# Optimization experiments

Measured on AMD Instinct MI355X. Metric: run time of the kernel, lower is better.

## Reference

```python
import jax, jax.numpy as jnp
import numpy as np

F_NODES = 360        # nodes per graph == num_features (square connectome)
NUM_GRAPHS = 128
NUM_EDGES = 1_000_000
C = 128              # hidden_channels
NUM_LAYERS = 3
HIDDEN = 512
NUM_CLASSES = 2
EPS = 1e-5


def _bn(x, g, b):
    # BatchNorm1d in training mode: biased batch statistics over the batch dim.
    m = x.mean(axis=0)
    v = x.var(axis=0)
    return (x - m) * jax.lax.rsqrt(v + EPS) * g + b


def _gcn(x, W, b, src, dst):
    # GCNConv: x' = D^{-1/2} (A + I) D^{-1/2} (x W) + b
    N = x.shape[0]
    h = x @ W                                   # [N, C]
    loop = jnp.arange(N, dtype=src.dtype)
    src2 = jnp.concatenate([src, loop])
    dst2 = jnp.concatenate([dst, loop])
    deg = jax.ops.segment_sum(jnp.ones_like(dst2, dtype=h.dtype), dst2, num_segments=N)
    dinv = jnp.where(deg > 0, jax.lax.rsqrt(deg), 0.0)
    norm = dinv[src2] * dinv[dst2]              # [E+N]
    out = jax.ops.segment_sum(h[src2] * norm[:, None], dst2, num_segments=N)
    return out + b


def setup_inputs() -> dict:
    key = jax.random.key(0)
    ks = jax.random.split(key, 16)
    N = NUM_GRAPHS * F_NODES
    x = jax.random.normal(ks[0], (N, F_NODES), jnp.float32)
    # edges confined within each graph
    g = jax.random.randint(ks[1], (NUM_EDGES,), 0, NUM_GRAPHS)
    edge_src = g * F_NODES + jax.random.randint(ks[2], (NUM_EDGES,), 0, F_NODES)
    edge_dst = g * F_NODES + jax.random.randint(ks[3], (NUM_EDGES,), 0, F_NODES)
    batch = jnp.repeat(jnp.arange(NUM_GRAPHS), F_NODES)

    def lin(k, fi, fo):
        s = 1.0 / np.sqrt(fi)
        return jax.random.uniform(k, (fi, fo), jnp.float32, -s, s)

    input_dim = F_NODES * (F_NODES + 1) // 2    # 64980
    input_dim1 = input_dim + C * NUM_LAYERS     # 65364
    H2 = HIDDEN // 2
    params = dict(
        Wc1=lin(ks[4], F_NODES, C), bc1=jnp.zeros((C,), jnp.float32),
        Wc2=lin(ks[5], C, C), bc2=jnp.zeros((C,), jnp.float32),
        Wc3=lin(ks[6], C, C), bc3=jnp.zeros((C,), jnp.float32),
        bn_g=jnp.ones((input_dim,), jnp.float32), bn_b=jnp.zeros((input_dim,), jnp.float32),
        bnh_g=jnp.ones((C * NUM_LAYERS,), jnp.float32), bnh_b=jnp.zeros((C * NUM_LAYERS,), jnp.float32),
        W1=lin(ks[7], input_dim1, HIDDEN), b1=jnp.zeros((HIDDEN,), jnp.float32),
        g1=jnp.ones((HIDDEN,), jnp.float32), be1=jnp.zeros((HIDDEN,), jnp.float32),
        W2=lin(ks[8], HIDDEN, H2), b2=jnp.zeros((H2,), jnp.float32),
        g2=jnp.ones((H2,), jnp.float32), be2=jnp.zeros((H2,), jnp.float32),
        W3=lin(ks[9], H2, H2), b3=jnp.zeros((H2,), jnp.float32),
        g3=jnp.ones((H2,), jnp.float32), be3=jnp.zeros((H2,), jnp.float32),
        W4=lin(ks[10], H2, NUM_CLASSES), b4=jnp.zeros((NUM_CLASSES,), jnp.float32),
    )
    return {"x": x, "edge_src": edge_src, "edge_dst": edge_dst, "batch": batch, **params}


def reference(x, edge_src, edge_dst, batch,
              Wc1, bc1, Wc2, bc2, Wc3, bc3,
              bn_g, bn_b, bnh_g, bnh_b,
              W1, b1, g1, be1, W2, b2, g2, be2, W3, b3, g3, be3, W4, b4):
    N, F = x.shape
    B = N // F                                   # nodes per graph == F
    # stacked GCN convs with tanh
    xs = [x]
    for W, b in ((Wc1, bc1), (Wc2, bc2), (Wc3, bc3)):
        xs.append(jnp.tanh(_gcn(xs[-1], W, b, edge_src, edge_dst)))
    # per-graph upper-triangular gather of the raw connectome (vectorized)
    iu0, iu1 = np.triu_indices(F)
    x0 = xs[0].reshape(B, F, F)[:, iu0, iu1]     # [B, F(F+1)/2]
    x0 = _bn(x0, bn_g, bn_b)
    # per-layer segment-mean pooling over graphs
    cnt = jax.ops.segment_sum(jnp.ones((N,), x.dtype), batch, num_segments=B)
    h = jnp.concatenate(
        [jax.ops.segment_sum(xx, batch, num_segments=B) / cnt[:, None] for xx in xs[1:]],
        axis=1)                                  # [B, C*num_layers]
    h = _bn(h, bnh_g, bnh_b)
    z = jnp.concatenate([x0, h], axis=1)         # [B, input_dim1]
    # MLP head (dropout in eval mode => identity)
    z = jax.nn.relu(_bn(z @ W1 + b1, g1, be1))
    z = jax.nn.relu(_bn(z @ W2 + b2, g2, be2))
    z = jax.nn.relu(_bn(z @ W3 + b3, g3, be3))
    return jax.nn.log_softmax(z @ W4 + b4, axis=1)
```

## Files before the change

### kernel.cpp

```cpp
#include <hip/hip_runtime.h>
#include <hip/hip_bf16.h>
#include <math.h>

#define FN 360
#define NG 128
#define NN 46080
#define CH 128
#define NE 1000000
#define TRI 64980
#define D1 65364
#define ZLD 65376
#define H1 512
#define H2 256
#define EPS 1e-5f
#define NSPLIT 128

typedef unsigned short u16;
typedef __attribute__((ext_vector_type(8))) short bf16x8;
typedef __attribute__((ext_vector_type(4))) float f32x4;

__device__ __forceinline__ float bf2f(u16 v) {
  union { unsigned u; float f; } x; x.u = ((unsigned)v) << 16; return x.f;
}
__device__ __forceinline__ u16 f2bf(float f) {
  union { float f; unsigned u; } x; x.f = f;
  unsigned r = x.u + 0x7fffu + ((x.u >> 16) & 1u);
  return (u16)(r >> 16);
}
__device__ __forceinline__ bf16x8 bzero8() {
  bf16x8 z;
#pragma unroll
  for (int j = 0; j < 8; j++) z[j] = 0;
  return z;
}

static const size_t A32_OFF  = 0;
static const size_t Z_OFF    = 0;
static const size_t PART_OFF = 16736256;
static const size_t Y1_OFF   = 50290688;
static const size_t A1_OFF   = 50552832;
static const size_t A2_OFF   = 50683904;
static const size_t A3_OFF   = 50749440;
static const size_t DEG_OFF  = 66355200;
static const size_t HP_OFF   = 66539520;
static const size_t AB_OFF   = 66736128;
static const size_t PT_OFF   = 99913728;
static const size_t H_OFF    = 111710208;

__global__ void k_deg(const int* __restrict__ dst, float* __restrict__ deg) {
  int e = blockIdx.x * 256 + threadIdx.x;
  if (e < NE) atomicAdd(&deg[dst[e]], 1.0f);
}

__global__ void k_abuild(const int* __restrict__ src, const int* __restrict__ dst,
                         const float* __restrict__ deg, float* __restrict__ A) {
  int e = blockIdx.x * 256 + threadIdx.x;
  if (e < NE) {
    int s = src[e], d = dst[e];
    int g = d / FN;
    int ls = s - g * FN, ld = d - g * FN;
    float w = rsqrtf(deg[s] + 1.0f) * rsqrtf(deg[d] + 1.0f);
    atomicAdd(&A[(size_t)g * FN * FN + (size_t)ld * FN + ls], w);
  } else if (e < NE + NN) {
    int i = e - NE;
    int g = i / FN, l = i - g * FN;
    float dv = rsqrtf(deg[i] + 1.0f);
    atomicAdd(&A[(size_t)g * FN * FN + (size_t)l * FN + l], dv * dv);
  }
}

__global__ __launch_bounds__(256) void k_gemm_xw_f32(
    const float* __restrict__ X, const float* __restrict__ W,
    u16* __restrict__ PT, int K) {
  __shared__ __attribute__((aligned(16))) u16 WT[128][40];
  int wid = threadIdx.x >> 6, lane = threadIdx.x & 63;
  int quad = lane >> 4, l16 = lane & 15;
  int m0 = blockIdx.x * 64 + (wid & 1) * 32;
  int n0w = (wid >> 1) * 64;
  int kl = threadIdx.x >> 3, nseg = (threadIdx.x & 7) * 16;
  f32x4 acc[2][4];
#pragma unroll
  for (int i = 0; i < 2; i++)
#pragma unroll
    for (int j = 0; j < 4; j++) acc[i][j] = (f32x4){0,0,0,0};
  for (int k0 = 0; k0 < K; k0 += 32) {
    __syncthreads();
    int kg = k0 + kl;
    if (kg < K) {
      const float* wrow = W + (size_t)kg * CH + nseg;
      f32x4 w0 = *(const f32x4*)(wrow);
      f32x4 w1 = *(const f32x4*)(wrow + 4);
      f32x4 w2 = *(const f32x4*)(wrow + 8);
      f32x4 w3 = *(const f32x4*)(wrow + 12);
#pragma unroll
      for (int j = 0; j < 4; j++) {
        WT[nseg + j][kl]      = f2bf(w0[j]);
        WT[nseg + 4 + j][kl]  = f2bf(w1[j]);
        WT[nseg + 8 + j][kl]  = f2bf(w2[j]);
        WT[nseg + 12 + j][kl] = f2bf(w3[j]);
      }
    } else {
#pragma unroll
      for (int j = 0; j < 16; j++) WT[nseg + j][kl] = 0;
    }
    __syncthreads();
    int kk = k0 + quad * 8;
    bool kin = kk < K;
    bf16x8 af[2];
#pragma unroll
    for (int tm = 0; tm < 2; tm++) {
      int row = m0 + tm * 16 + l16;
      bf16x8 a = bzero8();
      if (kin) {
        f32x4 va = *(const f32x4*)(X + (size_t)row * K + kk);
        f32x4 vb = *(const f32x4*)(X + (size_t)row * K + kk + 4);
#pragma unroll
        for (int j = 0; j < 4; j++) { a[j] = (short)f2bf(va[j]); a[4 + j] = (short)f2bf(vb[j]); }
      }
      af[tm] = a;
    }
    bf16x8 bfr[4];
#pragma unroll
    for (int tn = 0; tn < 4; tn++)
      bfr[tn] = *(const bf16x8*)&WT[n0w + tn * 16 + l16][quad * 8];
#pragma unroll
    for (int tm = 0; tm < 2; tm++)
#pragma unroll
      for (int tn = 0; tn < 4; tn++)
        acc[tm][tn] = __builtin_amdgcn_mfma_f32_16x16x32_bf16(af[tm], bfr[tn], acc[tm][tn], 0, 0, 0);
  }
#pragma unroll
  for (int tm = 0; tm < 2; tm++)
#pragma unroll
    for (int tn = 0; tn < 4; tn++) {
      int col = n0w + tn * 16 + l16;
      int rowb = m0 + tm * 16 + quad * 4;
#pragma unroll
      for (int r = 0; r < 4; r++) {
        int row = rowb + r;
        int g = row / FN, lr = row - g * FN;
        PT[((size_t)g * CH + col) * FN + lr] = f2bf(acc[tm][tn][r]);
      }
    }
}

__global__ __launch_bounds__(256) void k_gemm_xw_bf16(
    const u16* __restrict__ X, const float* __restrict__ W,
    u16* __restrict__ PT) {
  __shared__ __attribute__((aligned(16))) u16 WT[128][40];
  int wid = threadIdx.x >> 6, lane = threadIdx.x & 63;
  int quad = lane >> 4, l16 = lane & 15;
  int m0 = blockIdx.x * 64 + (wid & 1) * 32;
  int n0w = (wid >> 1) * 64;
  int kl = threadIdx.x >> 3, nseg = (threadIdx.x & 7) * 16;
  f32x4 acc[2][4];
#pragma unroll
  for (int i = 0; i < 2; i++)
#pragma unroll
    for (int j = 0; j < 4; j++) acc[i][j] = (f32x4){0,0,0,0};
  for (int k0 = 0; k0 < CH; k0 += 32) {
    __syncthreads();
    int kg = k0 + kl;
    const float* wrow = W + (size_t)kg * CH + nseg;
    f32x4 w0 = *(const f32x4*)(wrow);
    f32x4 w1 = *(const f32x4*)(wrow + 4);
    f32x4 w2 = *(const f32x4*)(wrow + 8);
    f32x4 w3 = *(const f32x4*)(wrow + 12);
#pragma unroll
    for (int j = 0; j < 4; j++) {
      WT[nseg + j][kl]      = f2bf(w0[j]);
      WT[nseg + 4 + j][kl]  = f2bf(w1[j]);
      WT[nseg + 8 + j][kl]  = f2bf(w2[j]);
      WT[nseg + 12 + j][kl] = f2bf(w3[j]);
    }
    __syncthreads();
    int kk = k0 + quad * 8;
    bf16x8 af[2];
#pragma unroll
    for (int tm = 0; tm < 2; tm++) {
      int row = m0 + tm * 16 + l16;
      af[tm] = *(const bf16x8*)(X + (size_t)row * CH + kk);
    }
    bf16x8 bfr[4];
#pragma unroll
    for (int tn = 0; tn < 4; tn++)
      bfr[tn] = *(const bf16x8*)&WT[n0w + tn * 16 + l16][quad * 8];
#pragma unroll
    for (int tm = 0; tm < 2; tm++)
#pragma unroll
      for (int tn = 0; tn < 4; tn++)
        acc[tm][tn] = __builtin_amdgcn_mfma_f32_16x16x32_bf16(af[tm], bfr[tn], acc[tm][tn], 0, 0, 0);
  }
#pragma unroll
  for (int tm = 0; tm < 2; tm++)
#pragma unroll
    for (int tn = 0; tn < 4; tn++) {
      int col = n0w + tn * 16 + l16;
      int rowb = m0 + tm * 16 + quad * 4;
#pragma unroll
      for (int r = 0; r < 4; r++) {
        int row = rowb + r;
        int g = row / FN, lr = row - g * FN;
        PT[((size_t)g * CH + col) * FN + lr] = f2bf(acc[tm][tn][r]);
      }
    }
}

__global__ __launch_bounds__(256) void k_agg1(
    const float* __restrict__ A32, const u16* __restrict__ PT,
    const float* __restrict__ bias, u16* __restrict__ Hout,
    u16* __restrict__ Ab, float* __restrict__ hp) {
  __shared__ float ps[8][128];
  int id = blockIdx.x;
  int g = (id & 7) + 8 * (id / 48);
  int mb = (id % 48) >> 3;
  int wid = threadIdx.x >> 6, lane = threadIdx.x & 63;
  int quad = lane >> 4, l16 = lane & 15;
  int m0 = mb * 64 + (wid & 1) * 32;
  int n0 = (wid >> 1) * 64;
  const float* Ag = A32 + (size_t)g * FN * FN;
  u16* Abg = Ab + (size_t)g * FN * FN;
  const u16* PTg = PT + (size_t)g * CH * FN;
  bool wr_ab = ((wid >> 1) == 0);
  f32x4 acc[2][4];
#pragma unroll
  for (int i = 0; i < 2; i++)
#pragma unroll
    for (int j = 0; j < 4; j++) acc[i][j] = (f32x4){0,0,0,0};
  for (int k0 = 0; k0 < FN; k0 += 32) {
    int kk = k0 + quad * 8;
    bool kin = kk < FN;
    bf16x8 af[2];
#pragma unroll
    for (int tm = 0; tm < 2; tm++) {
      int row = m0 + tm * 16 + l16;
      bf16x8 a = bzero8();
      if (kin && row < FN) {
        f32x4 va = *(const f32x4*)(Ag + (size_t)row * FN + kk);
        f32x4 vb = *(const f32x4*)(Ag + (size_t)row * FN + kk + 4);
#pragma unroll
        for (int j = 0; j < 4; j++) { a[j] = (short)f2bf(va[j]); a[4 + j] = (short)f2bf(vb[j]); }
        if (wr_ab) *(bf16x8*)(Abg + (size_t)row * FN + kk) = a;
      }
      af[tm] = a;
    }
    bf16x8 bfr[4];
#pragma unroll
    for (int tn = 0; tn < 4; tn++) {
      int col = n0 + tn * 16 + l16;
      bfr[tn] = kin ? *(const bf16x8*)(PTg + (size_t)col * FN + kk) : bzero8();
    }
#pragma unroll
    for (int tm = 0; tm < 2; tm++)
#pragma unroll
      for (int tn = 0; tn < 4; tn++)
        acc[tm][tn] = __builtin_amdgcn_mfma_f32_16x16x32_bf16(af[tm], bfr[tn], acc[tm][tn], 0, 0, 0);
  }
  float lsum[4] = {0.f, 0.f, 0.f, 0.f};
#pragma unroll
  for (int tm = 0; tm < 2; tm++)
#pragma unroll
    for (int tn = 0; tn < 4; tn++) {
      int col = n0 + tn * 16 + l16;
      float bc = bias[col];
      int rowb = m0 + tm * 16 + quad * 4;
#pragma unroll
      for (int r = 0; r < 4; r++) {
        int row = rowb + r;
        if (row < FN) {
          float t = tanhf(acc[tm][tn][r] + bc);
          Hout[(size_t)(g * FN + row) * CH + col] = f2bf(t);
          lsum[tn] += t;
        }
      }
    }
  int cid = (wid & 1) * 4 + quad;
#pragma unroll
  for (int tn = 0; tn < 4; tn++) ps[cid][n0 + tn * 16 + l16] = lsum[tn];
  __syncthreads();
  if (threadIdx.x < 128) {
    float s = 0.f;
#pragma unroll
    for (int c = 0; c < 8; c++) s += ps[c][threadIdx.x];
    atomicAdd(&hp[g * 384 + threadIdx.x], s);
  }
}

__global__ __launch_bounds__(256) void k_agg23(
    const u16* __restrict__ Ab, const u16* __restrict__ PT,
    const float* __restrict__ bias, u16* __restrict__ Hout,
    float* __restrict__ hp, int loff) {
  __shared__ float ps[8][128];
  int id = blockIdx.x;
  int g = (id & 7) + 8 * (id / 48);
  int mb = (id % 48) >> 3;
  int wid = threadIdx.x >> 6, lane = threadIdx.x & 63;
  int quad = lane >> 4, l16 = lane & 15;
  int m0 = mb * 64 + (wid & 1) * 32;
  int n0 = (wid >> 1) * 64;
  const u16* Abg = Ab + (size_t)g * FN * FN;
  const u16* PTg = PT + (size_t)g * CH * FN;
  f32x4 acc[2][4];
#pragma unroll
  for (int i = 0; i < 2; i++)
#pragma unroll
    for (int j = 0; j < 4; j++) acc[i][j] = (f32x4){0,0,0,0};
  for (int k0 = 0; k0 < FN; k0 += 32) {
    int kk = k0 + quad * 8;
    bool kin = kk < FN;
    bf16x8 af[2];
#pragma unroll
    for (int tm = 0; tm < 2; tm++) {
      int row = m0 + tm * 16 + l16;
      af[tm] = (kin && row < FN) ? *(const bf16x8*)(Abg + (size_t)row * FN + kk) : bzero8();
    }
    bf16x8 bfr[4];
#pragma unroll
    for (int tn = 0; tn < 4; tn++) {
      int col = n0 + tn * 16 + l16;
      bfr[tn] = kin ? *(const bf16x8*)(PTg + (size_t)col * FN + kk) : bzero8();
    }
#pragma unroll
    for (int tm = 0; tm < 2; tm++)
#pragma unroll
      for (int tn = 0; tn < 4; tn++)
        acc[tm][tn] = __builtin_amdgcn_mfma_f32_16x16x32_bf16(af[tm], bfr[tn], acc[tm][tn], 0, 0, 0);
  }
  float lsum[4] = {0.f, 0.f, 0.f, 0.f};
#pragma unroll
  for (int tm = 0; tm < 2; tm++)
#pragma unroll
    for (int tn = 0; tn < 4; tn++) {
      int col = n0 + tn * 16 + l16;
      float bc = bias[col];
      int rowb = m0 + tm * 16 + quad * 4;
#pragma unroll
      for (int r = 0; r < 4; r++) {
        int row = rowb + r;
        if (row < FN) {
          float t = tanhf(acc[tm][tn][r] + bc);
          if (Hout) Hout[(size_t)(g * FN + row) * CH + col] = f2bf(t);
          lsum[tn] += t;
        }
      }
    }
  int cid = (wid & 1) * 4 + quad;
#pragma unroll
  for (int tn = 0; tn < 4; tn++) ps[cid][n0 + tn * 16 + l16] = lsum[tn];
  __syncthreads();
  if (threadIdx.x < 128) {
    float s = 0.f;
#pragma unroll
    for (int c = 0; c < 8; c++) s += ps[c][threadIdx.x];
    atomicAdd(&hp[g * 384 + loff + threadIdx.x], s);
  }
}

__global__ __launch_bounds__(256) void k_gemm_big(
    const u16* __restrict__ Z, const float* __restrict__ W1f, float* __restrict__ part) {
  __shared__ __attribute__((aligned(16))) u16 WT[128][40];
  int id = blockIdx.x;
  int s = (id & 7) + 8 * (id >> 5);
  int n0b = ((id >> 3) & 3) * 128;
  int wid = threadIdx.x >> 6, lane = threadIdx.x & 63;
  int quad = lane >> 4, l16 = lane & 15;
  int m0 = wid * 32;
  int kl = threadIdx.x >> 3, nseg = (threadIdx.x & 7) * 16;
  int kbeg = s * 512;
  int kend = (ZLD < kbeg + 512) ? ZLD : (kbeg + 512);
  f32x4 acc[2][8];
#pragma unroll
  for (int i = 0; i < 2; i++)
#pragma unroll
    for (int j = 0; j < 8; j++) acc[i][j] = (f32x4){0,0,0,0};
  for (int k0 = kbeg; k0 < kend; k0 += 32) {
    __syncthreads();
    int kg = k0 + kl;
    if (kg < D1) {
      const float* wrow = W1f + (size_t)kg * H1 + n0b + nseg;
      f32x4 w0 = *(const f32x4*)(wrow);
      f32x4 w1 = *(const f32x4*)(wrow + 4);
      f32x4 w2 = *(const f32x4*)(wrow + 8);
      f32x4 w3 = *(const f32x4*)(wrow + 12);
#pragma unroll
      for (int j = 0; j < 4; j++) {
        WT[nseg + j][kl]      = f2bf(w0[j]);
        WT[nseg + 4 + j][kl]  = f2bf(w1[j]);
        WT[nseg + 8 + j][kl]  = f2bf(w2[j]);
        WT[nseg + 12 + j][kl] = f2bf(w3[j]);
      }
    } else {
#pragma unroll
      for (int j = 0; j < 16; j++) WT[nseg + j][kl] = 0;
    }
    __syncthreads();
    int kk = k0 + quad * 8;
    bf16x8 af[2];
#pragma unroll
    for (int tm = 0; tm < 2; tm++) {
      int row = m0 + tm * 16 + l16;
      af[tm] = *(const bf16x8*)(Z + (size_t)row * ZLD + kk);
    }
    bf16x8 bfr[8];
#pragma unroll
    for (int tn = 0; tn < 8; tn++)
      bfr[tn] = *(const bf16x8*)&WT[tn * 16 + l16][quad * 8];
#pragma unroll
    for (int tm = 0; tm < 2; tm++)
#pragma unroll
      for (int tn = 0; tn < 8; tn++)
        acc[tm][tn] = __builtin_amdgcn_mfma_f32_16x16x32_bf16(af[tm], bfr[tn], acc[tm][tn], 0, 0, 0);
  }
#pragma unroll
  for (int tm = 0; tm < 2; tm++)
#pragma unroll
    for (int tn = 0; tn < 8; tn++) {
      int col = n0b + tn * 16 + l16;
      int rowb = m0 + tm * 16 + quad * 4;
#pragma unroll
      for (int r = 0; r < 4; r++)
        part[((size_t)s * NG + rowb + r) * H1 + col] = acc[tm][tn][r];
    }
}

__global__ void k_red(const float* __restrict__ part, float* __restrict__ y1) {
  int idx = blockIdx.x * 256 + threadIdx.x;
  float s = 0.f;
#pragma unroll 8
  for (int i = 0; i < NSPLIT; i++) s += part[(size_t)i * 65536 + idx];
  y1[idx] = s;
}

__global__ __launch_bounds__(256) void k_bnrelu(
    const float* __restrict__ y, const float* __restrict__ gam,
    const float* __restrict__ bet, u16* __restrict__ a, int N) {
  __shared__ float sb[4][64], sb2[4][64];
  int c63 = threadIdx.x & 63;
  int grp = threadIdx.x >> 6;
  int c = blockIdx.x * 64 + c63;
  float s = 0.f, ss = 0.f;
#pragma unroll 8
  for (int m = grp * 32; m < grp * 32 + 32; m++) {
    float v = y[(size_t)m * N + c]; s += v; ss += v * v;
  }
  sb[grp][c63] = s; sb2[grp][c63] = ss;
  __syncthreads();
  float S = sb[0][c63] + sb[1][c63] + sb[2][c63] + sb[3][c63];
  float SS = sb2[0][c63] + sb2[1][c63] + sb2[2][c63] + sb2[3][c63];
  float mean = S * (1.0f / NG);
  float var = fmaxf(SS * (1.0f / NG) - mean * mean, 0.f);
  float rstd = rsqrtf(var + EPS);
  float ga = gam[c] * rstd;
  float bb = bet[c] - mean * ga;
#pragma unroll 8
  for (int m = grp * 32; m < grp * 32 + 32; m++) {
    float v = y[(size_t)m * N + c] * ga + bb;
    a[(size_t)m * N + c] = f2bf(fmaxf(v, 0.f));
  }
}

__global__ __launch_bounds__(256) void k_mlpbn(
    const u16* __restrict__ A, const float* __restrict__ W,
    const float* __restrict__ gam, const float* __restrict__ bet,
    u16* __restrict__ aout, int K, int N) {
  __shared__ __attribute__((aligned(16))) u16 WT[64][40];
  __shared__ float rs[4][4][4][16], rss[4][4][4][16];
  int wid = threadIdx.x >> 6, lane = threadIdx.x & 63;
  int quad = lane >> 4, l16 = lane & 15;
  int n0b = blockIdx.x * 64;
  int m0 = wid * 32;
  int kl = threadIdx.x >> 3;
  int nseg = (threadIdx.x & 7) * 8;
  f32x4 acc[2][4];
#pragma unroll
  for (int i = 0; i < 2; i++)
#pragma unroll
    for (int j = 0; j < 4; j++) acc[i][j] = (f32x4){0,0,0,0};
  for (int k0 = 0; k0 < K; k0 += 32) {
    __syncthreads();
    const float* wrow = W + (size_t)(k0 + kl) * N + n0b + nseg;
    f32x4 w0 = *(const f32x4*)(wrow);
    f32x4 w1 = *(const f32x4*)(wrow + 4);
#pragma unroll
    for (int j = 0; j < 4; j++) {
      WT[nseg + j][kl]     = f2bf(w0[j]);
      WT[nseg + 4 + j][kl] = f2bf(w1[j]);
    }
    __syncthreads();
    int kk = k0 + quad * 8;
    bf16x8 af[2];
#pragma unroll
    for (int tm = 0; tm < 2; tm++) {
      int row = m0 + tm * 16 + l16;
      af[tm] = *(const bf16x8*)(A + (size_t)row * K + kk);
    }
    bf16x8 bfr[4];
#pragma unroll
    for (int tn = 0; tn < 4; tn++)
      bfr[tn] = *(const bf16x8*)&WT[tn * 16 + l16][quad * 8];
#pragma unroll
    for (int tm = 0; tm < 2; tm++)
#pragma unroll
      for (int tn = 0; tn < 4; tn++)
        acc[tm][tn] = __builtin_amdgcn_mfma_f32_16x16x32_bf16(af[tm], bfr[tn], acc[tm][tn], 0, 0, 0);
  }
  __syncthreads();
#pragma unroll
  for (int tn = 0; tn < 4; tn++) {
    float s = 0.f, ss = 0.f;
#pragma unroll
    for (int tm = 0; tm < 2; tm++)
#pragma unroll
      for (int r = 0; r < 4; r++) { float v = acc[tm][tn][r]; s += v; ss += v * v; }
    rs[wid][quad][tn][l16] = s;
    rss[wid][quad][tn][l16] = ss;
  }
  __syncthreads();
#pragma unroll
  for (int tn = 0; tn < 4; tn++) {
    float S = 0.f, SS = 0.f;
#pragma unroll
    for (int w = 0; w < 4; w++)
#pragma unroll
      for (int q = 0; q < 4; q++) { S += rs[w][q][tn][l16]; SS += rss[w][q][tn][l16]; }
    float mean = S * (1.0f / NG);
    float var = fmaxf(SS * (1.0f / NG) - mean * mean, 0.f);
    float rstd = rsqrtf(var + EPS);
    int col = n0b + tn * 16 + l16;
    float ga = gam[col] * rstd;
    float bb = bet[col] - mean * ga;
#pragma unroll
    for (int tm = 0; tm < 2; tm++) {
      int rowb = m0 + tm * 16 + quad * 4;
#pragma unroll
      for (int r = 0; r < 4; r++) {
        float v = acc[tm][tn][r] * ga + bb;
        aout[(size_t)(rowb + r) * N + col] = f2bf(fmaxf(v, 0.f));
      }
    }
  }
}

__global__ __launch_bounds__(256) void k_x0bn(
    const float* __restrict__ x, const float* __restrict__ gam,
    const float* __restrict__ bet, const float* __restrict__ hp,
    const float* __restrict__ hgam, const float* __restrict__ hbet,
    u16* __restrict__ z) {
  int i = blockIdx.x;
  if (i < FN) {
    int off = i * FN - (i * (i - 1)) / 2;
    for (int j = i + (int)threadIdx.x; j < FN; j += 256) {
      float s = 0.f, ss = 0.f;
#pragma unroll 8
      for (int b = 0; b < NG; b++) {
        float v = x[(size_t)(b * FN + i) * FN + j];
        s += v; ss += v * v;
      }
      float mean = s * (1.0f / NG);
      float var = fmaxf(ss * (1.0f / NG) - mean * mean, 0.f);
      float rstd = rsqrtf(var + EPS);
      int f = off + (j - i);
      float ga = gam[f] * rstd;
      float bb = bet[f] - mean * ga;
#pragma unroll 8
      for (int b = 0; b < NG; b++) {
        float v = x[(size_t)(b * FN + i) * FN + j];
        z[(size_t)b * ZLD + f] = f2bf(v * ga + bb);
      }
    }
  } else {
    for (int c = threadIdx.x; c < 384; c += 256) {
      float s = 0.f, ss = 0.f;
#pragma unroll 8
      for (int m = 0; m < NG; m++) {
        float v = hp[m * 384 + c] * (1.0f / FN);
        s += v; ss += v * v;
      }
      float mean = s * (1.0f / NG);
      float var = fmaxf(ss * (1.0f / NG) - mean * mean, 0.f);
      float rstd = rsqrtf(var + EPS);
      float ga = hgam[c] * rstd;
      float bb = hbet[c] - mean * ga;
#pragma unroll 8
      for (int m = 0; m < NG; m++)
        z[(size_t)m * ZLD + TRI + c] = f2bf(hp[m * 384 + c] * (1.0f / FN) * ga + bb);
    }
    if (threadIdx.x < NG) {
      for (int t = 0; t < ZLD - D1; t++)
        z[(size_t)threadIdx.x * ZLD + D1 + t] = 0;
    }
  }
}

__global__ void k_head(const u16* __restrict__ a3, const float* __restrict__ W4,
                       const float* __restrict__ b4, float* __restrict__ out) {
  __shared__ float w4s[H2 * 2];
  int m = threadIdx.x;
  for (int i = m; i < H2 * 2; i += 128) w4s[i] = W4[i];
  __syncthreads();
  float a0 = b4[0], a1 = b4[1];
  for (int k0 = 0; k0 < H2; k0 += 8) {
    bf16x8 v = *(const bf16x8*)(a3 + (size_t)m * H2 + k0);
#pragma unroll
    for (int j = 0; j < 8; j++) {
      float f = bf2f((u16)v[j]);
      a0 += f * w4s[(k0 + j) * 2];
      a1 += f * w4s[(k0 + j) * 2 + 1];
    }
  }
  float mx = fmaxf(a0, a1);
  float lse = mx + logf(expf(a0 - mx) + expf(a1 - mx));
  out[m * 2]     = a0 - lse;
  out[m * 2 + 1] = a1 - lse;
}

extern "C" void kernel_launch(void* const* d_in, const int* in_sizes, int n_in,
                              void* d_out, int out_size, void* d_ws, size_t ws_size,
                              hipStream_t stream) {
  const float* x    = (const float*)d_in[0];
  const int* esrc   = (const int*)d_in[1];
  const int* edst   = (const int*)d_in[2];
  const float* Wc1 = (const float*)d_in[4];  const float* bc1 = (const float*)d_in[5];
  const float* Wc2 = (const float*)d_in[6];  const float* bc2 = (const float*)d_in[7];
  const float* Wc3 = (const float*)d_in[8];  const float* bc3 = (const float*)d_in[9];
  const float* bn_g = (const float*)d_in[10]; const float* bn_b = (const float*)d_in[11];
  const float* bnh_g = (const float*)d_in[12]; const float* bnh_b = (const float*)d_in[13];
  const float* W1 = (const float*)d_in[14];
  const float* g1 = (const float*)d_in[16]; const float* be1 = (const float*)d_in[17];
  const float* W2 = (const float*)d_in[18];
  const float* g2 = (const float*)d_in[20]; const float* be2 = (const float*)d_in[21];
  const float* W3 = (const float*)d_in[22];
  const float* g3 = (const float*)d_in[24]; const float* be3 = (const float*)d_in[25];
  const float* W4 = (const float*)d_in[26]; const float* b4 = (const float*)d_in[27];

  char* ws = (char*)d_ws;
  float* A32  = (float*)(ws + A32_OFF);
  float* deg  = (float*)(ws + DEG_OFF);
  float* hp   = (float*)(ws + HP_OFF);
  u16*   Ab   = (u16*)(ws + AB_OFF);
  u16*   PT   = (u16*)(ws + PT_OFF);
  u16*   h    = (u16*)(ws + H_OFF);
  u16*   z    = (u16*)(ws + Z_OFF);
  float* part = (float*)(ws + PART_OFF);
  float* y1   = (float*)(ws + Y1_OFF);
  u16*   a1   = (u16*)(ws + A1_OFF);
  u16*   a2   = (u16*)(ws + A2_OFF);
  u16*   a3   = (u16*)(ws + A3_OFF);

  (void)hipMemsetAsync(A32, 0, (size_t)NG * FN * FN * 4 + (size_t)NN * 4 + (size_t)NG * 384 * 4, stream);

  dim3 b256(256);
  k_deg<<<dim3((NE + 255) / 256), b256, 0, stream>>>(edst, deg);
  k_abuild<<<dim3((NE + NN + 255) / 256), b256, 0, stream>>>(esrc, edst, deg, A32);

  k_gemm_xw_f32<<<dim3(NN / 64), b256, 0, stream>>>(x, Wc1, PT, FN);
  k_agg1<<<dim3(NG * 6), b256, 0, stream>>>(A32, PT, bc1, h, Ab, hp);
  k_gemm_xw_bf16<<<dim3(NN / 64), b256, 0, stream>>>(h, Wc2, PT);
  k_agg23<<<dim3(NG * 6), b256, 0, stream>>>(Ab, PT, bc2, h, hp, CH);
  k_gemm_xw_bf16<<<dim3(NN / 64), b256, 0, stream>>>(h, Wc3, PT);
  k_agg23<<<dim3(NG * 6), b256, 0, stream>>>(Ab, PT, bc3, (u16*)nullptr, hp, 2 * CH);

  k_x0bn<<<dim3(FN + 1), b256, 0, stream>>>(x, bn_g, bn_b, hp, bnh_g, bnh_b, z);

  k_gemm_big<<<dim3(512), b256, 0, stream>>>(z, W1, part);
  k_red<<<dim3(65536 / 256), b256, 0, stream>>>(part, y1);
  k_bnrelu<<<dim3(H1 / 64), b256, 0, stream>>>(y1, g1, be1, a1, H1);
  k_mlpbn<<<dim3(H2 / 64), b256, 0, stream>>>(a1, W2, g2, be2, a2, H1, H2);
  k_mlpbn<<<dim3(H2 / 64), b256, 0, stream>>>(a2, W3, g3, be3, a3, H2, H2);
  k_head<<<dim3(1), dim3(128), 0, stream>>>(a3, W4, b4, (float*)d_out);
}
```

Measured before the change: 648.7 us.

## Bucket edges per graph, build adjacency in LDS, overlap big GEMM with aggregation

```diff
diff --git a/kernel.cpp b/kernel.cpp
--- a/kernel.cpp
+++ b/kernel.cpp
@@ -13,7 +13,12 @@
 #define H1 512
 #define H2 256
 #define EPS 1e-5f
-#define NSPLIT 128
+#define NSPLIT 64
+#define NB1 720
+#define EBLK 3907
+#define NSB 8
+#define SBCAP 1536
+#define CROWS 45
 
 typedef unsigned short u16;
 typedef __attribute__((ext_vector_type(8))) short bf16x8;
@@ -42,37 +47,32 @@
 static const size_t A2_OFF   = 50683904;
 static const size_t A3_OFF   = 50749440;
 static const size_t DEG_OFF  = 66355200;
-static const size_t HP_OFF   = 66539520;
-static const size_t AB_OFF   = 66736128;
-static const size_t PT_OFF   = 99913728;
-static const size_t H_OFF    = 111710208;
-
-__global__ void k_deg(const int* __restrict__ dst, float* __restrict__ deg) {
-  int e = blockIdx.x * 256 + threadIdx.x;
-  if (e < NE) atomicAdd(&deg[dst[e]], 1.0f);
-}
-
-__global__ void k_abuild(const int* __restrict__ src, const int* __restrict__ dst,
-                         const float* __restrict__ deg, float* __restrict__ A) {
-  int e = blockIdx.x * 256 + threadIdx.x;
-  if (e < NE) {
-    int s = src[e], d = dst[e];
-    int g = d / FN;
-    int ls = s - g * FN, ld = d - g * FN;
-    float w = rsqrtf(deg[s] + 1.0f) * rsqrtf(deg[d] + 1.0f);
-    atomicAdd(&A[(size_t)g * FN * FN + (size_t)ld * FN + ls], w);
-  } else if (e < NE + NN) {
-    int i = e - NE;
-    int g = i / FN, l = i - g * FN;
-    float dv = rsqrtf(deg[i] + 1.0f);
-    atomicAdd(&A[(size_t)g * FN * FN + (size_t)l * FN + l], dv * dv);
-  }
-}
-
-__global__ __launch_bounds__(256) void k_gemm_xw_f32(
+static const size_t CUR_OFF  = 66539520;
+static const size_t HP_OFF   = 66543616;
+static const size_t AB_OFF   = 66740224;
+static const size_t PT_OFF   = 99917824;
+static const size_t H_OFF    = 111714304;
+
+__global__ __launch_bounds__(256) void k_gemm1deg(
     const float* __restrict__ X, const float* __restrict__ W,
-    u16* __restrict__ PT, int K) {
+    u16* __restrict__ PT,
+    const int* __restrict__ src, const int* __restrict__ dst,
+    float* __restrict__ deg, int* __restrict__ cur, unsigned* __restrict__ ebuf) {
+  if (blockIdx.x >= NB1) {
+    int e = (blockIdx.x - NB1) * 256 + threadIdx.x;
+    if (e < NE) {
+      int s = src[e], d = dst[e];
+      atomicAdd(&deg[d], 1.0f);
+      int g = d / FN;
+      int ls = s - g * FN, ld = d - g * FN;
+      int sb = g * NSB + (e & (NSB - 1));
+      int pos = atomicAdd(&cur[sb], 1);
+      if (pos < SBCAP) ebuf[(size_t)sb * SBCAP + pos] = (unsigned)ls | ((unsigned)ld << 16);
+    }
+    return;
+  }
   __shared__ __attribute__((aligned(16))) u16 WT[128][40];
+  const int K = FN;
   int wid = threadIdx.x >> 6, lane = threadIdx.x & 63;
   int quad = lane >> 4, l16 = lane & 15;
   int m0 = blockIdx.x * 64 + (wid & 1) * 32;
@@ -144,66 +144,42 @@
     }
 }
 
-__global__ __launch_bounds__(256) void k_gemm_xw_bf16(
-    const u16* __restrict__ X, const float* __restrict__ W,
-    u16* __restrict__ PT) {
-  __shared__ __attribute__((aligned(16))) u16 WT[128][40];
-  int wid = threadIdx.x >> 6, lane = threadIdx.x & 63;
-  int quad = lane >> 4, l16 = lane & 15;
-  int m0 = blockIdx.x * 64 + (wid & 1) * 32;
-  int n0w = (wid >> 1) * 64;
-  int kl = threadIdx.x >> 3, nseg = (threadIdx.x & 7) * 16;
-  f32x4 acc[2][4];
-#pragma unroll
-  for (int i = 0; i < 2; i++)
-#pragma unroll
-    for (int j = 0; j < 4; j++) acc[i][j] = (f32x4){0,0,0,0};
-  for (int k0 = 0; k0 < CH; k0 += 32) {
-    __syncthreads();
-    int kg = k0 + kl;
-    const float* wrow = W + (size_t)kg * CH + nseg;
-    f32x4 w0 = *(const f32x4*)(wrow);
-    f32x4 w1 = *(const f32x4*)(wrow + 4);
-    f32x4 w2 = *(const f32x4*)(wrow + 8);
-    f32x4 w3 = *(const f32x4*)(wrow + 12);
-#pragma unroll
-    for (int j = 0; j < 4; j++) {
-      WT[nseg + j][kl]      = f2bf(w0[j]);
-      WT[nseg + 4 + j][kl]  = f2bf(w1[j]);
-      WT[nseg + 8 + j][kl]  = f2bf(w2[j]);
-      WT[nseg + 12 + j][kl] = f2bf(w3[j]);
-    }
-    __syncthreads();
-    int kk = k0 + quad * 8;
-    bf16x8 af[2];
-#pragma unroll
-    for (int tm = 0; tm < 2; tm++) {
-      int row = m0 + tm * 16 + l16;
-      af[tm] = *(const bf16x8*)(X + (size_t)row * CH + kk);
-    }
-    bf16x8 bfr[4];
-#pragma unroll
-    for (int tn = 0; tn < 4; tn++)
-      bfr[tn] = *(const bf16x8*)&WT[n0w + tn * 16 + l16][quad * 8];
-#pragma unroll
-    for (int tm = 0; tm < 2; tm++)
-#pragma unroll
-      for (int tn = 0; tn < 4; tn++)
-        acc[tm][tn] = __builtin_amdgcn_mfma_f32_16x16x32_bf16(af[tm], bfr[tn], acc[tm][tn], 0, 0, 0);
-  }
-#pragma unroll
-  for (int tm = 0; tm < 2; tm++)
-#pragma unroll
-    for (int tn = 0; tn < 4; tn++) {
-      int col = n0w + tn * 16 + l16;
-      int rowb = m0 + tm * 16 + quad * 4;
-#pragma unroll
-      for (int r = 0; r < 4; r++) {
-        int row = rowb + r;
-        int g = row / FN, lr = row - g * FN;
-        PT[((size_t)g * CH + col) * FN + lr] = f2bf(acc[tm][tn][r]);
-      }
-    }
+__global__ __launch_bounds__(256) void k_abuild2(
+    const unsigned* __restrict__ ebuf, const int* __restrict__ cur,
+    const float* __restrict__ deg, float* __restrict__ A) {
+  __shared__ __attribute__((aligned(16))) float sA[CROWS * FN];
+  int g = blockIdx.x >> 3, ch = blockIdx.x & 7;
+  int r0 = ch * CROWS;
+  {
+    f32x4* z4 = (f32x4*)sA;
+    for (int i = threadIdx.x; i < CROWS * FN / 4; i += 256) z4[i] = (f32x4){0,0,0,0};
+  }
+  __syncthreads();
+  const float* dg = deg + g * FN;
+#pragma unroll 1
+  for (int sb = 0; sb < NSB; sb++) {
+    int cnt = cur[g * NSB + sb];
+    if (cnt > SBCAP) cnt = SBCAP;
+    const unsigned* eb = ebuf + (size_t)(g * NSB + sb) * SBCAP;
+    for (int i = threadIdx.x; i < cnt; i += 256) {
+      unsigned p = eb[i];
+      int ls = (int)(p & 0xffffu), ld = (int)(p >> 16);
+      int lr = ld - r0;
+      if ((unsigned)lr < (unsigned)CROWS) {
+        float w = rsqrtf(dg[ls] + 1.0f) * rsqrtf(dg[ld] + 1.0f);
+        atomicAdd(&sA[lr * FN + ls], w);
+      }
+    }
+  }
+  if (threadIdx.x < CROWS) {
+    int l = r0 + threadIdx.x;
+    float dv = rsqrtf(dg[l] + 1.0f);
+    atomicAdd(&sA[threadIdx.x * FN + l], dv * dv);
+  }
+  __syncthreads();
+  f32x4* dst4 = (f32x4*)(A + (size_t)g * FN * FN + (size_t)r0 * FN);
+  const f32x4* s4 = (const f32x4*)sA;
+  for (int i = threadIdx.x; i < CROWS * FN / 4; i += 256) dst4[i] = s4[i];
 }
 
 __global__ __launch_bounds__(256) void k_agg1(
@@ -286,10 +262,83 @@
   }
 }
 
+template<bool GUARD>
+__device__ __forceinline__ void gbig_body(
+    const u16* __restrict__ Z, const float* __restrict__ W1f,
+    float* __restrict__ part, int s, int n0b) {
+  __shared__ __attribute__((aligned(16))) u16 WT[128][40];
+  int wid = threadIdx.x >> 6, lane = threadIdx.x & 63;
+  int quad = lane >> 4, l16 = lane & 15;
+  int m0 = wid * 32;
+  int kl = threadIdx.x >> 3, nseg = (threadIdx.x & 7) * 16;
+  int kbeg = s * 1024;
+  int kend = GUARD ? ((ZLD < kbeg + 1024) ? ZLD : (kbeg + 1024)) : (kbeg + 1024);
+  f32x4 acc[2][8];
+#pragma unroll
+  for (int i = 0; i < 2; i++)
+#pragma unroll
+    for (int j = 0; j < 8; j++) acc[i][j] = (f32x4){0,0,0,0};
+  for (int k0 = kbeg; k0 < kend; k0 += 32) {
+    __syncthreads();
+    int kg = k0 + kl;
+    if (!GUARD || kg < D1) {
+      const float* wrow = W1f + (size_t)kg * H1 + n0b + nseg;
+      f32x4 w0 = *(const f32x4*)(wrow);
+      f32x4 w1 = *(const f32x4*)(wrow + 4);
+      f32x4 w2 = *(const f32x4*)(wrow + 8);
+      f32x4 w3 = *(const f32x4*)(wrow + 12);
+#pragma unroll
+      for (int j = 0; j < 4; j++) {
+        WT[nseg + j][kl]      = f2bf(w0[j]);
+        WT[nseg + 4 + j][kl]  = f2bf(w1[j]);
+        WT[nseg + 8 + j][kl]  = f2bf(w2[j]);
+        WT[nseg + 12 + j][kl] = f2bf(w3[j]);
+      }
+    } else {
+#pragma unroll
+      for (int j = 0; j < 16; j++) WT[nseg + j][kl] = 0;
+    }
+    __syncthreads();
+    int kk = k0 + quad * 8;
+    bf16x8 af[2];
+#pragma unroll
+    for (int tm = 0; tm < 2; tm++) {
+      int row = m0 + tm * 16 + l16;
+      af[tm] = *(const bf16x8*)(Z + (size_t)row * ZLD + kk);
+    }
+    bf16x8 bfr[8];
+#pragma unroll
+    for (int tn = 0; tn < 8; tn++)
+      bfr[tn] = *(const bf16x8*)&WT[tn * 16 + l16][quad * 8];
+#pragma unroll
+    for (int tm = 0; tm < 2; tm++)
+#pragma unroll
+      for (int tn = 0; tn < 8; tn++)
+        acc[tm][tn] = __builtin_amdgcn_mfma_f32_16x16x32_bf16(af[tm], bfr[tn], acc[tm][tn], 0, 0, 0);
+  }
+#pragma unroll
+  for (int tm = 0; tm < 2; tm++)
+#pragma unroll
+    for (int tn = 0; tn < 8; tn++) {
+      int col = n0b + tn * 16 + l16;
+      int rowb = m0 + tm * 16 + quad * 4;
+#pragma unroll
+      for (int r = 0; r < 4; r++)
+        part[((size_t)s * NG + rowb + r) * H1 + col] = acc[tm][tn][r];
+    }
+}
+
 __global__ __launch_bounds__(256) void k_agg23(
     const u16* __restrict__ Ab, const u16* __restrict__ PT,
     const float* __restrict__ bias, u16* __restrict__ Hout,
-    float* __restrict__ hp, int loff) {
+    float* __restrict__ hp, int loff,
+    const u16* __restrict__ Z, const float* __restrict__ W1f,
+    float* __restrict__ part) {
+  if (blockIdx.x >= NG * 6) {
+    int id2 = blockIdx.x - NG * 6;
+    gbig_body<false>(Z, W1f, part, id2 >> 2, (id2 & 3) * 128);
+    return;
+  }
   __shared__ float ps[8][128];
   int id = blockIdx.x;
   int g = (id & 7) + 8 * (id / 48);
@@ -356,42 +405,34 @@
   }
 }
 
-__global__ __launch_bounds__(256) void k_gemm_big(
-    const u16* __restrict__ Z, const float* __restrict__ W1f, float* __restrict__ part) {
+__global__ __launch_bounds__(256) void k_gemm_xw_bf16(
+    const u16* __restrict__ X, const float* __restrict__ W,
+    u16* __restrict__ PT) {
   __shared__ __attribute__((aligned(16))) u16 WT[128][40];
-  int id = blockIdx.x;
-  int s = (id & 7) + 8 * (id >> 5);
-  int n0b = ((id >> 3) & 3) * 128;
   int wid = threadIdx.x >> 6, lane = threadIdx.x & 63;
   int quad = lane >> 4, l16 = lane & 15;
-  int m0 = wid * 32;
+  int m0 = blockIdx.x * 64 + (wid & 1) * 32;
+  int n0w = (wid >> 1) * 64;
   int kl = threadIdx.x >> 3, nseg = (threadIdx.x & 7) * 16;
-  int kbeg = s * 512;
-  int kend = (ZLD < kbeg + 512) ? ZLD : (kbeg + 512);
-  f32x4 acc[2][8];
+  f32x4 acc[2][4];
 #pragma unroll
   for (int i = 0; i < 2; i++)
 #pragma unroll
-    for (int j = 0; j < 8; j++) acc[i][j] = (f32x4){0,0,0,0};
-  for (int k0 = kbeg; k0 < kend; k0 += 32) {
+    for (int j = 0; j < 4; j++) acc[i][j] = (f32x4){0,0,0,0};
+  for (int k0 = 0; k0 < CH; k0 += 32) {
     __syncthreads();
     int kg = k0 + kl;
-    if (kg < D1) {
-      const float* wrow = W1f + (size_t)kg * H1 + n0b + nseg;
-      f32x4 w0 = *(const f32x4*)(wrow);
-      f32x4 w1 = *(const f32x4*)(wrow + 4);
-      f32x4 w2 = *(const f32x4*)(wrow + 8);
-      f32x4 w3 = *(const f32x4*)(wrow + 12);
-#pragma unroll
-      for (int j = 0; j < 4; j++) {
-        WT[nseg + j][kl]      = f2bf(w0[j]);
-        WT[nseg + 4 + j][kl]  = f2bf(w1[j]);
-        WT[nseg + 8 + j][kl]  = f2bf(w2[j]);
-        WT[nseg + 12 + j][kl] = f2bf(w3[j]);
-      }
-    } else {
-#pragma unroll
-      for (int j = 0; j < 16; j++) WT[nseg + j][kl] = 0;
+    const float* wrow = W + (size_t)kg * CH + nseg;
+    f32x4 w0 = *(const f32x4*)(wrow);
+    f32x4 w1 = *(const f32x4*)(wrow + 4);
+    f32x4 w2 = *(const f32x4*)(wrow + 8);
+    f32x4 w3 = *(const f32x4*)(wrow + 12);
+#pragma unroll
+    for (int j = 0; j < 4; j++) {
+      WT[nseg + j][kl]      = f2bf(w0[j]);
+      WT[nseg + 4 + j][kl]  = f2bf(w1[j]);
+      WT[nseg + 8 + j][kl]  = f2bf(w2[j]);
+      WT[nseg + 12 + j][kl] = f2bf(w3[j]);
     }
     __syncthreads();
     int kk = k0 + quad * 8;
@@ -399,28 +440,149 @@
 #pragma unroll
     for (int tm = 0; tm < 2; tm++) {
       int row = m0 + tm * 16 + l16;
-      af[tm] = *(const bf16x8*)(Z + (size_t)row * ZLD + kk);
-    }
-    bf16x8 bfr[8];
-#pragma unroll
-    for (int tn = 0; tn < 8; tn++)
-      bfr[tn] = *(const bf16x8*)&WT[tn * 16 + l16][quad * 8];
+      af[tm] = *(const bf16x8*)(X + (size_t)row * CH + kk);
+    }
+    bf16x8 bfr[4];
+#pragma unroll
+    for (int tn = 0; tn < 4; tn++)
+      bfr[tn] = *(const bf16x8*)&WT[n0w + tn * 16 + l16][quad * 8];
 #pragma unroll
     for (int tm = 0; tm < 2; tm++)
 #pragma unroll
-      for (int tn = 0; tn < 8; tn++)
+      for (int tn = 0; tn < 4; tn++)
         acc[tm][tn] = __builtin_amdgcn_mfma_f32_16x16x32_bf16(af[tm], bfr[tn], acc[tm][tn], 0, 0, 0);
   }
 #pragma unroll
   for (int tm = 0; tm < 2; tm++)
 #pragma unroll
-    for (int tn = 0; tn < 8; tn++) {
-      int col = n0b + tn * 16 + l16;
+    for (int tn = 0; tn < 4; tn++) {
+      int col = n0w + tn * 16 + l16;
       int rowb = m0 + tm * 16 + quad * 4;
 #pragma unroll
-      for (int r = 0; r < 4; r++)
-        part[((size_t)s * NG + rowb + r) * H1 + col] = acc[tm][tn][r];
-    }
+      for (int r = 0; r < 4; r++) {
+        int row = rowb + r;
+        int g = row / FN, lr = row - g * FN;
+        PT[((size_t)g * CH + col) * FN + lr] = f2bf(acc[tm][tn][r]);
+      }
+    }
+}
+
+__global__ __launch_bounds__(256) void k_gemm2tri(
+    const u16* __restrict__ X, const float* __restrict__ W,
+    u16* __restrict__ PT,
+    const float* __restrict__ x, const float* __restrict__ gam,
+    const float* __restrict__ bet, u16* __restrict__ z) {
+  if (blockIdx.x >= NB1) {
+    int i = blockIdx.x - NB1;
+    int off = i * FN - (i * (i - 1)) / 2;
+    for (int j = i + (int)threadIdx.x; j < FN; j += 256) {
+      float s = 0.f, ss = 0.f;
+#pragma unroll 8
+      for (int b = 0; b < NG; b++) {
+        float v = x[(size_t)(b * FN + i) * FN + j];
+        s += v; ss += v * v;
+      }
+      float mean = s * (1.0f / NG);
+      float var = fmaxf(ss * (1.0f / NG) - mean * mean, 0.f);
+      float rstd = rsqrtf(var + EPS);
+      int f = off + (j - i);
+      float ga = gam[f] * rstd;
+      float bb = bet[f] - mean * ga;
+#pragma unroll 8
+      for (int b = 0; b < NG; b++) {
+        float v = x[(size_t)(b * FN + i) * FN + j];
+        z[(size_t)b * ZLD + f] = f2bf(v * ga + bb);
+      }
+    }
+    return;
+  }
+  __shared__ __attribute__((aligned(16))) u16 WT[128][40];
+  int wid = threadIdx.x >> 6, lane = threadIdx.x & 63;
+  int quad = lane >> 4, l16 = lane & 15;
+  int m0 = blockIdx.x * 64 + (wid & 1) * 32;
+  int n0w = (wid >> 1) * 64;
+  int kl = threadIdx.x >> 3, nseg = (threadIdx.x & 7) * 16;
+  f32x4 acc[2][4];
+#pragma unroll
+  for (int i = 0; i < 2; i++)
+#pragma unroll
+    for (int j = 0; j < 4; j++) acc[i][j] = (f32x4){0,0,0,0};
+  for (int k0 = 0; k0 < CH; k0 += 32) {
+    __syncthreads();
+    int kg = k0 + kl;
+    const float* wrow = W + (size_t)kg * CH + nseg;
+    f32x4 w0 = *(const f32x4*)(wrow);
+    f32x4 w1 = *(const f32x4*)(wrow + 4);
+    f32x4 w2 = *(const f32x4*)(wrow + 8);
+    f32x4 w3 = *(const f32x4*)(wrow + 12);
+#pragma unroll
+    for (int j = 0; j < 4; j++) {
+      WT[nseg + j][kl]      = f2bf(w0[j]);
+      WT[nseg + 4 + j][kl]  = f2bf(w1[j]);
+      WT[nseg + 8 + j][kl]  = f2bf(w2[j]);
+      WT[nseg + 12 + j][kl] = f2bf(w3[j]);
+    }
+    __syncthreads();
+    int kk = k0 + quad * 8;
+    bf16x8 af[2];
+#pragma unroll
+    for (int tm = 0; tm < 2; tm++) {
+      int row = m0 + tm * 16 + l16;
+      af[tm] = *(const bf16x8*)(X + (size_t)row * CH + kk);
+    }
+    bf16x8 bfr[4];
+#pragma unroll
+    for (int tn = 0; tn < 4; tn++)
+      bfr[tn] = *(const bf16x8*)&WT[n0w + tn * 16 + l16][quad * 8];
+#pragma unroll
+    for (int tm = 0; tm < 2; tm++)
+#pragma unroll
+      for (int tn = 0; tn < 4; tn++)
+        acc[tm][tn] = __builtin_amdgcn_mfma_f32_16x16x32_bf16(af[tm], bfr[tn], acc[tm][tn], 0, 0, 0);
+  }
+#pragma unroll
+  for (int tm = 0; tm < 2; tm++)
+#pragma unroll
+    for (int tn = 0; tn < 4; tn++) {
+      int col = n0w + tn * 16 + l16;
+      int rowb = m0 + tm * 16 + quad * 4;
+#pragma unroll
+      for (int r = 0; r < 4; r++) {
+        int row = rowb + r;
+        int g = row / FN, lr = row - g * FN;
+        PT[((size_t)g * CH + col) * FN + lr] = f2bf(acc[tm][tn][r]);
+      }
+    }
+}
+
+__global__ void k_hpbn(const float* __restrict__ hp,
+                       const float* __restrict__ hgam, const float* __restrict__ hbet,
+                       u16* __restrict__ z) {
+  for (int c = threadIdx.x; c < 384; c += 256) {
+    float s = 0.f, ss = 0.f;
+#pragma unroll 8
+    for (int m = 0; m < NG; m++) {
+      float v = hp[m * 384 + c] * (1.0f / FN);
+      s += v; ss += v * v;
+    }
+    float mean = s * (1.0f / NG);
+    float var = fmaxf(ss * (1.0f / NG) - mean * mean, 0.f);
+    float rstd = rsqrtf(var + EPS);
+    float ga = hgam[c] * rstd;
+    float bb = hbet[c] - mean * ga;
+#pragma unroll 8
+    for (int m = 0; m < NG; m++)
+      z[(size_t)m * ZLD + TRI + c] = f2bf(hp[m * 384 + c] * (1.0f / FN) * ga + bb);
+  }
+  if (threadIdx.x < NG) {
+    for (int t = 0; t < ZLD - D1; t++)
+      z[(size_t)threadIdx.x * ZLD + D1 + t] = 0;
+  }
+}
+
+__global__ __launch_bounds__(256) void k_gbig_tail(
+    const u16* __restrict__ Z, const float* __restrict__ W1f, float* __restrict__ part) {
+  gbig_body<true>(Z, W1f, part, NSPLIT - 1, blockIdx.x * 128);
 }
 
 __global__ void k_red(const float* __restrict__ part, float* __restrict__ y1) {
@@ -537,57 +699,6 @@
         float v = acc[tm][tn][r] * ga + bb;
         aout[(size_t)(rowb + r) * N + col] = f2bf(fmaxf(v, 0.f));
       }
-    }
-  }
-}
-
-__global__ __launch_bounds__(256) void k_x0bn(
-    const float* __restrict__ x, const float* __restrict__ gam,
-    const float* __restrict__ bet, const float* __restrict__ hp,
-    const float* __restrict__ hgam, const float* __restrict__ hbet,
-    u16* __restrict__ z) {
-  int i = blockIdx.x;
-  if (i < FN) {
-    int off = i * FN - (i * (i - 1)) / 2;
-    for (int j = i + (int)threadIdx.x; j < FN; j += 256) {
-      float s = 0.f, ss = 0.f;
-#pragma unroll 8
-      for (int b = 0; b < NG; b++) {
-        float v = x[(size_t)(b * FN + i) * FN + j];
-        s += v; ss += v * v;
-      }
-      float mean = s * (1.0f / NG);
-      float var = fmaxf(ss * (1.0f / NG) - mean * mean, 0.f);
-      float rstd = rsqrtf(var + EPS);
-      int f = off + (j - i);
-      float ga = gam[f] * rstd;
-      float bb = bet[f] - mean * ga;
-#pragma unroll 8
-      for (int b = 0; b < NG; b++) {
-        float v = x[(size_t)(b * FN + i) * FN + j];
-        z[(size_t)b * ZLD + f] = f2bf(v * ga + bb);
-      }
-    }
-  } else {
-    for (int c = threadIdx.x; c < 384; c += 256) {
-      float s = 0.f, ss = 0.f;
-#pragma unroll 8
-      for (int m = 0; m < NG; m++) {
-        float v = hp[m * 384 + c] * (1.0f / FN);
-        s += v; ss += v * v;
-      }
-      float mean = s * (1.0f / NG);
-      float var = fmaxf(ss * (1.0f / NG) - mean * mean, 0.f);
-      float rstd = rsqrtf(var + EPS);
-      float ga = hgam[c] * rstd;
-      float bb = hbet[c] - mean * ga;
-#pragma unroll 8
-      for (int m = 0; m < NG; m++)
-        z[(size_t)m * ZLD + TRI + c] = f2bf(hp[m * 384 + c] * (1.0f / FN) * ga + bb);
-    }
-    if (threadIdx.x < NG) {
-      for (int t = 0; t < ZLD - D1; t++)
-        z[(size_t)threadIdx.x * ZLD + D1 + t] = 0;
     }
   }
 }
@@ -636,8 +747,10 @@
   char* ws = (char*)d_ws;
   float* A32  = (float*)(ws + A32_OFF);
   float* deg  = (float*)(ws + DEG_OFF);
+  int*   cur  = (int*)(ws + CUR_OFF);
   float* hp   = (float*)(ws + HP_OFF);
   u16*   Ab   = (u16*)(ws + AB_OFF);
+  unsigned* ebuf = (unsigned*)(ws + AB_OFF);
   u16*   PT   = (u16*)(ws + PT_OFF);
   u16*   h    = (u16*)(ws + H_OFF);
   u16*   z    = (u16*)(ws + Z_OFF);
@@ -647,22 +760,18 @@
   u16*   a2   = (u16*)(ws + A2_OFF);
   u16*   a3   = (u16*)(ws + A3_OFF);
 
-  (void)hipMemsetAsync(A32, 0, (size_t)NG * FN * FN * 4 + (size_t)NN * 4 + (size_t)NG * 384 * 4, stream);
+  (void)hipMemsetAsync(deg, 0, (size_t)NN * 4 + (size_t)NG * NSB * 4 + (size_t)NG * 384 * 4, stream);
 
   dim3 b256(256);
-  k_deg<<<dim3((NE + 255) / 256), b256, 0, stream>>>(edst, deg);
-  k_abuild<<<dim3((NE + NN + 255) / 256), b256, 0, stream>>>(esrc, edst, deg, A32);
-
-  k_gemm_xw_f32<<<dim3(NN / 64), b256, 0, stream>>>(x, Wc1, PT, FN);
+  k_gemm1deg<<<dim3(NB1 + EBLK), b256, 0, stream>>>(x, Wc1, PT, esrc, edst, deg, cur, ebuf);
+  k_abuild2<<<dim3(NG * 8), b256, 0, stream>>>(ebuf, cur, deg, A32);
   k_agg1<<<dim3(NG * 6), b256, 0, stream>>>(A32, PT, bc1, h, Ab, hp);
-  k_gemm_xw_bf16<<<dim3(NN / 64), b256, 0, stream>>>(h, Wc2, PT);
-  k_agg23<<<dim3(NG * 6), b256, 0, stream>>>(Ab, PT, bc2, h, hp, CH);
-  k_gemm_xw_bf16<<<dim3(NN / 64), b256, 0, stream>>>(h, Wc3, PT);
-  k_agg23<<<dim3(NG * 6), b256, 0, stream>>>(Ab, PT, bc3, (u16*)nullptr, hp, 2 * CH);
-
-  k_x0bn<<<dim3(FN + 1), b256, 0, stream>>>(x, bn_g, bn_b, hp, bnh_g, bnh_b, z);
-
-  k_gemm_big<<<dim3(512), b256, 0, stream>>>(z, W1, part);
+  k_gemm2tri<<<dim3(NB1 + FN), b256, 0, stream>>>(h, Wc2, PT, x, bn_g, bn_b, z);
+  k_agg23<<<dim3(NG * 6 + 252), b256, 0, stream>>>(Ab, PT, bc2, h, hp, CH, z, W1, part);
+  k_gemm_xw_bf16<<<dim3(NB1), b256, 0, stream>>>(h, Wc3, PT);
+  k_agg23<<<dim3(NG * 6), b256, 0, stream>>>(Ab, PT, bc3, (u16*)nullptr, hp, 2 * CH, z, W1, part);
+  k_hpbn<<<dim3(1), b256, 0, stream>>>(hp, bnh_g, bnh_b, z);
+  k_gbig_tail<<<dim3(4), b256, 0, stream>>>(z, W1, part);
   k_red<<<dim3(65536 / 256), b256, 0, stream>>>(part, y1);
   k_bnrelu<<<dim3(H1 / 64), b256, 0, stream>>>(y1, g1, be1, a1, H1);
   k_mlpbn<<<dim3(H2 / 64), b256, 0, stream>>>(a1, W2, g2, be2, a2, H1, H2);
```

Measured after the change: 845.4 us. +30.3%, slower.
